# Performance work log

Hardware: AMD Instinct MI355X
Metric: run time of the kernel (lower is better)

Reference implementation:

```python
import jax, jax.numpy as jnp
import numpy as np

N_NODES = 100000
N_EDGES = 1600000
NODE_DIM = 128
EDGE_DIM = 32
GLOBAL_DIM = 64
HIDDEN_DIM = 256
N_GRAPHS = 512
IN_DIM = NODE_DIM + EDGE_DIM + GLOBAL_DIM  # 224


def setup_inputs() -> dict:
    key = jax.random.key(0)
    ks = jax.random.split(key, 10)
    x = jax.random.normal(ks[0], (N_NODES, NODE_DIM), dtype=jnp.float32)
    edge_index = jax.random.randint(ks[1], (2, N_EDGES), 0, N_NODES, dtype=jnp.int64)
    edge_attr = jax.random.normal(ks[2], (N_EDGES, EDGE_DIM), dtype=jnp.float32)
    u = jax.random.normal(ks[3], (N_GRAPHS, GLOBAL_DIM), dtype=jnp.float32)
    batch = jnp.sort(jax.random.randint(ks[4], (N_NODES,), 0, N_GRAPHS, dtype=jnp.int64))
    s1 = 1.0 / np.sqrt(IN_DIM)
    s2 = 1.0 / np.sqrt(HIDDEN_DIM)
    W1 = jax.random.uniform(ks[5], (IN_DIM, HIDDEN_DIM), jnp.float32, -s1, s1)
    b1 = jnp.zeros((HIDDEN_DIM,), jnp.float32)
    W2 = jax.random.uniform(ks[6], (HIDDEN_DIM, HIDDEN_DIM), jnp.float32, -s2, s2)
    b2 = jnp.zeros((HIDDEN_DIM,), jnp.float32)
    W3 = jax.random.uniform(ks[7], (HIDDEN_DIM, GLOBAL_DIM), jnp.float32, -s2, s2)
    b3 = jnp.zeros((GLOBAL_DIM,), jnp.float32)
    return {"x": x, "edge_index": edge_index, "edge_attr": edge_attr, "u": u,
            "batch": batch, "W1": W1, "b1": b1, "W2": W2, "b2": b2, "W3": W3, "b3": b3}


def _scatter_mean(vals, seg_ids, num_segments):
    # vals: [M, D], seg_ids: [M] -> [num_segments, D]
    sums = jax.ops.segment_sum(vals, seg_ids, num_segments=num_segments)
    cnt = jax.ops.segment_sum(jnp.ones((vals.shape[0],), vals.dtype), seg_ids,
                              num_segments=num_segments)
    return sums / jnp.maximum(cnt, 1.0)[:, None]


def reference(x, edge_index, edge_attr, u, batch, W1, b1, W2, b2, W3, b3):
    B = u.shape[0]
    node_mean = _scatter_mean(x, batch, B)                      # [B, node_dim]
    edge_seg = batch[edge_index[0]]                             # [E]
    edge_mean = _scatter_mean(edge_attr, edge_seg, B)           # [B, edge_dim]
    out = jnp.concatenate([node_mean, edge_mean, u], axis=1)    # [B, in_dim]
    h = jax.nn.relu(out @ W1 + b1)
    h = jax.nn.relu(h @ W2 + b2)
    return h @ W3 + b3                                          # [B, global_dim]
```

## Files before the change

### kernel.cpp

```cpp
#include <hip/hip_runtime.h>
#include <hip/hip_bf16.h>

#define N_NODES    100000
#define N_EDGES    1600000
#define NODE_DIM   128
#define EDGE_DIM   32
#define GLOBAL_DIM 64
#define HIDDEN_DIM 256
#define N_GRAPHS   512
#define IN_DIM     224
#define ROW33      33

#define EDGE_BLKS  256
#define EDGE_CH    (N_EDGES / EDGE_BLKS)
#define SLOTSZ     (N_GRAPHS * ROW33)
#define GPB        2
#define PD         4

#define FXS   1048576.0f
#define FXINV (1.0f / 1048576.0f)

#define WS_NSUM   0
#define WS_NCNT   (WS_NSUM + N_GRAPHS * NODE_DIM)
#define WS_ESLOT  (WS_NCNT + N_GRAPHS)

__global__ __launch_bounds__(1024, 8) void bulk(const float* __restrict__ eattr,
                                                const int* __restrict__ eidx,
                                                const float* __restrict__ x,
                                                const int* __restrict__ batch,
                                                int* __restrict__ eslot,
                                                float* __restrict__ nsum,
                                                float* __restrict__ ncnt) {
    __shared__ int ssum[SLOTSZ];
    const int t = threadIdx.x;

    if (blockIdx.x < EDGE_BLKS) {
        for (int i = t; i < SLOTSZ; i += 1024) ssum[i] = 0;
        __syncthreads();

        const float4* eattr4 = reinterpret_cast<const float4*>(eattr);
        const int p  = t & 7;
        const int e0 = blockIdx.x * EDGE_CH + (t >> 3);
        const int e1 = blockIdx.x * EDGE_CH + EDGE_CH;

        int    sQ[PD];
        float4 vQ[PD];
        int    iQ[PD];
#pragma unroll
        for (int k = 0; k < PD; ++k) {
            const int ek = e0 + k * 128;
            const int idx = eidx[ek];
            sQ[k] = batch[idx];
            vQ[k] = eattr4[(size_t)ek * 8 + p];
            iQ[k] = eidx[min(ek + PD * 128, N_EDGES - 1)];
        }

        for (int e = e0; e < e1; e += PD * 128) {
#pragma unroll
            for (int k = 0; k < PD; ++k) {
                const int ek = e + k * 128;
                if (ek < e1) {
                    const int s = sQ[k];
                    const float4 v = vQ[k];
                    const int ef = ek + PD * 128;
                    sQ[k] = batch[iQ[k]];
                    vQ[k] = (ef < e1) ? eattr4[(size_t)ef * 8 + p]
                                      : float4{0.f, 0.f, 0.f, 0.f};
                    iQ[k] = eidx[min(ek + 2 * PD * 128, N_EDGES - 1)];
                    const int b = s * ROW33 + p * 4;
                    atomicAdd(&ssum[b + 0], __float2int_rn(v.x * FXS));
                    atomicAdd(&ssum[b + 1], __float2int_rn(v.y * FXS));
                    atomicAdd(&ssum[b + 2], __float2int_rn(v.z * FXS));
                    atomicAdd(&ssum[b + 3], __float2int_rn(v.w * FXS));
                    if (p == 0) atomicAdd(&ssum[s * ROW33 + 32], 1);
                }
            }
        }
        __syncthreads();

        int* gs = eslot + (size_t)blockIdx.x * SLOTSZ;
        for (int i = t; i < SLOTSZ; i += 1024) gs[i] = ssum[i];
    } else {
        const int g = blockIdx.x - EDGE_BLKS;
        __shared__ int sb[2];
        if (t < 2) {
            const int target = g + t;
            int lo = 0, hi = N_NODES;
            while (lo < hi) {
                const int mid = (lo + hi) >> 1;
                if (batch[mid] < target) lo = mid + 1; else hi = mid;
            }
            sb[t] = lo;
        }
        __syncthreads();
        const int s0 = sb[0], e0 = sb[1];

        const int dq = t & 31;
        const int off = t >> 5;
        float4 a0 = float4{0.f, 0.f, 0.f, 0.f}, a1 = a0;
        int r = s0 + off;
        for (; r + 32 < e0; r += 64) {
            const float4 v0 = *reinterpret_cast<const float4*>(x + (size_t)(r     ) * NODE_DIM + dq * 4);
            const float4 v1 = *reinterpret_cast<const float4*>(x + (size_t)(r + 32) * NODE_DIM + dq * 4);
            a0.x += v0.x; a0.y += v0.y; a0.z += v0.z; a0.w += v0.w;
            a1.x += v1.x; a1.y += v1.y; a1.z += v1.z; a1.w += v1.w;
        }
        for (; r < e0; r += 32) {
            const float4 v = *reinterpret_cast<const float4*>(x + (size_t)r * NODE_DIM + dq * 4);
            a0.x += v.x; a0.y += v.y; a0.z += v.z; a0.w += v.w;
        }
        a0.x += a1.x; a0.y += a1.y; a0.z += a1.z; a0.w += a1.w;

        float4* part4 = reinterpret_cast<float4*>(ssum);
        part4[t] = a0;
        __syncthreads();
        if (t < 32) {
            float4 s = float4{0.f, 0.f, 0.f, 0.f};
#pragma unroll 32
            for (int k = 0; k < 32; ++k) {
                const float4 v = part4[t + 32 * k];
                s.x += v.x; s.y += v.y; s.z += v.z; s.w += v.w;
            }
            reinterpret_cast<float4*>(nsum)[(size_t)g * 32 + t] = s;
        }
        if (t == 0) ncnt[g] = fmaxf((float)(e0 - s0), 1.f);
    }
}

__global__ __launch_bounds__(256) void finalize_mlp(const float* __restrict__ nsum,
                                                    const float* __restrict__ ncnt,
                                                    const int* __restrict__ eslot,
                                                    const float* __restrict__ u,
                                                    const float* __restrict__ W1, const float* __restrict__ b1,
                                                    const float* __restrict__ W2, const float* __restrict__ b2,
                                                    const float* __restrict__ W3, const float* __restrict__ b3,
                                                    float* __restrict__ out) {
    const int g0 = blockIdx.x * GPB;
    const int t = threadIdx.x;
    __shared__ float fs[GPB * IN_DIM];
    __shared__ long long redll[256];
    __shared__ long long redcnt[8];
    __shared__ float h[GPB][HIDDEN_DIM];
    __shared__ float h2[GPB][HIDDEN_DIM];
    __shared__ float red[GPB][256];
    __shared__ float s_ecnt[GPB];

    {
        const int col = t & 63, part = t >> 6;
        const int g = col >> 5, d = col & 31;
        long long s = 0;
#pragma unroll 8
        for (int sl = part * 64; sl < part * 64 + 64; ++sl)
            s += eslot[(size_t)sl * SLOTSZ + (size_t)(g0 + g) * ROW33 + d];
        redll[t] = s;
    }
    if (t < 8) {
        const int g = t & 1, part = t >> 1;
        long long c = 0;
#pragma unroll 8
        for (int sl = part * 64; sl < part * 64 + 64; ++sl)
            c += eslot[(size_t)sl * SLOTSZ + (size_t)(g0 + g) * ROW33 + 32];
        redcnt[t] = c;
    }
    __syncthreads();
    if (t < GPB)
        s_ecnt[t] = fmaxf((float)(redcnt[t] + redcnt[t + 2] + redcnt[t + 4] + redcnt[t + 6]), 1.f);

    {
        const int g = t >> 7, d = t & 127;
        fs[g * IN_DIM + d] = nsum[(size_t)(g0 + g) * NODE_DIM + d] / ncnt[g0 + g];
    }
    __syncthreads();
    if (t < 64) {
        const long long tot = redll[t] + redll[t + 64] + redll[t + 128] + redll[t + 192];
        const int g = t >> 5, d = t & 31;
        fs[g * IN_DIM + NODE_DIM + d] = ((float)tot * FXINV) / s_ecnt[g];
    } else if (t < 192) {
        const int i = t - 64, g = i >> 6, c = i & 63;
        fs[g * IN_DIM + NODE_DIM + EDGE_DIM + c] = u[(size_t)(g0 + g) * GLOBAL_DIM + c];
    }
    __syncthreads();

    float acc0, acc1;
    const float bb1 = b1[t];
    acc0 = acc1 = bb1;
    for (int k = 0; k < IN_DIM; ++k) {
        const float w = W1[k * HIDDEN_DIM + t];
        acc0 = fmaf(fs[k], w, acc0);
        acc1 = fmaf(fs[IN_DIM + k], w, acc1);
    }
    h[0][t] = fmaxf(acc0, 0.f); h[1][t] = fmaxf(acc1, 0.f);
    __syncthreads();

    const float bb2 = b2[t];
    acc0 = acc1 = bb2;
    for (int k = 0; k < HIDDEN_DIM; ++k) {
        const float w = W2[k * HIDDEN_DIM + t];
        acc0 = fmaf(h[0][k], w, acc0);
        acc1 = fmaf(h[1][k], w, acc1);
    }
    h2[0][t] = fmaxf(acc0, 0.f); h2[1][t] = fmaxf(acc1, 0.f);
    __syncthreads();

    const int c3 = t & 63, q = t >> 6;
    acc0 = acc1 = 0.f;
    for (int k = q * 64; k < q * 64 + 64; ++k) {
        const float w = W3[k * GLOBAL_DIM + c3];
        acc0 = fmaf(h2[0][k], w, acc0);
        acc1 = fmaf(h2[1][k], w, acc1);
    }
    red[0][t] = acc0; red[1][t] = acc1;
    __syncthreads();
    if (t < GPB * GLOBAL_DIM) {
        const int g = t >> 6, c = t & 63;
        out[(size_t)(g0 + g) * GLOBAL_DIM + c] = red[g][c] + red[g][c + 64] +
                                                 red[g][c + 128] + red[g][c + 192] + b3[c];
    }
}

extern "C" void kernel_launch(void* const* d_in, const int* in_sizes, int n_in,
                              void* d_out, int out_size, void* d_ws, size_t ws_size,
                              hipStream_t stream) {
    const float* x         = (const float*)d_in[0];
    const int*   edge_idx  = (const int*)d_in[1];
    const float* edge_attr = (const float*)d_in[2];
    const float* u         = (const float*)d_in[3];
    const int*   batch     = (const int*)d_in[4];
    const float* W1 = (const float*)d_in[5];
    const float* b1 = (const float*)d_in[6];
    const float* W2 = (const float*)d_in[7];
    const float* b2 = (const float*)d_in[8];
    const float* W3 = (const float*)d_in[9];
    const float* b3 = (const float*)d_in[10];
    float* out = (float*)d_out;

    int* ws32 = (int*)d_ws;
    float* nsum  = (float*)(ws32 + WS_NSUM);
    float* ncnt  = (float*)(ws32 + WS_NCNT);
    int*   eslot = ws32 + WS_ESLOT;

    bulk<<<EDGE_BLKS + N_GRAPHS, 1024, 0, stream>>>(edge_attr, edge_idx, x, batch,
                                                    eslot, nsum, ncnt);
    finalize_mlp<<<N_GRAPHS / GPB, 256, 0, stream>>>(nsum, ncnt, eslot, u,
                                                     W1, b1, W2, b2, W3, b3, out);
}
```

Before: 81.35 us.

## Stage per-edge segment ids in LDS before edge accumulation loop

Each edge block now first resolves batch[eidx[e]] for its whole chunk with coalesced, independent gathers and stores the segment ids as 16-bit values in shared memory. The main loop then reads segment ids from LDS and only streams edge attributes, replacing the hand-rolled register prefetch queue with a simple unrolled loop. This separates the dependent two-level gather from the atomic accumulation so the gather latency is not exposed in the hot loop. In exchange it adds about 12.5 KB of LDS per block, an extra barrier phase, and drops the occupancy hint from launch bounds.

Result: slower. 84.28 us (+3.6%).

```diff
diff --git a/kernel.cpp b/kernel.cpp
--- a/kernel.cpp
+++ b/kernel.cpp
@@ -15,7 +15,6 @@
 #define EDGE_CH    (N_EDGES / EDGE_BLKS)
 #define SLOTSZ     (N_GRAPHS * ROW33)
 #define GPB        2
-#define PD         4
 
 #define FXS   1048576.0f
 #define FXINV (1.0f / 1048576.0f)
@@ -24,57 +23,37 @@
 #define WS_NCNT   (WS_NSUM + N_GRAPHS * NODE_DIM)
 #define WS_ESLOT  (WS_NCNT + N_GRAPHS)
 
-__global__ __launch_bounds__(1024, 8) void bulk(const float* __restrict__ eattr,
-                                                const int* __restrict__ eidx,
-                                                const float* __restrict__ x,
-                                                const int* __restrict__ batch,
-                                                int* __restrict__ eslot,
-                                                float* __restrict__ nsum,
-                                                float* __restrict__ ncnt) {
+__global__ __launch_bounds__(1024) void bulk(const float* __restrict__ eattr,
+                                             const int* __restrict__ eidx,
+                                             const float* __restrict__ x,
+                                             const int* __restrict__ batch,
+                                             int* __restrict__ eslot,
+                                             float* __restrict__ nsum,
+                                             float* __restrict__ ncnt) {
     __shared__ int ssum[SLOTSZ];
+    __shared__ unsigned short seg_lds[EDGE_CH];
     const int t = threadIdx.x;
 
     if (blockIdx.x < EDGE_BLKS) {
+        const int ebase = blockIdx.x * EDGE_CH;
+
         for (int i = t; i < SLOTSZ; i += 1024) ssum[i] = 0;
+        for (int i = t; i < EDGE_CH; i += 1024)
+            seg_lds[i] = (unsigned short)batch[eidx[ebase + i]];
         __syncthreads();
 
         const float4* eattr4 = reinterpret_cast<const float4*>(eattr);
-        const int p  = t & 7;
-        const int e0 = blockIdx.x * EDGE_CH + (t >> 3);
-        const int e1 = blockIdx.x * EDGE_CH + EDGE_CH;
-
-        int    sQ[PD];
-        float4 vQ[PD];
-        int    iQ[PD];
-#pragma unroll
-        for (int k = 0; k < PD; ++k) {
-            const int ek = e0 + k * 128;
-            const int idx = eidx[ek];
-            sQ[k] = batch[idx];
-            vQ[k] = eattr4[(size_t)ek * 8 + p];
-            iQ[k] = eidx[min(ek + PD * 128, N_EDGES - 1)];
-        }
-
-        for (int e = e0; e < e1; e += PD * 128) {
-#pragma unroll
-            for (int k = 0; k < PD; ++k) {
-                const int ek = e + k * 128;
-                if (ek < e1) {
-                    const int s = sQ[k];
-                    const float4 v = vQ[k];
-                    const int ef = ek + PD * 128;
-                    sQ[k] = batch[iQ[k]];
-                    vQ[k] = (ef < e1) ? eattr4[(size_t)ef * 8 + p]
-                                      : float4{0.f, 0.f, 0.f, 0.f};
-                    iQ[k] = eidx[min(ek + 2 * PD * 128, N_EDGES - 1)];
-                    const int b = s * ROW33 + p * 4;
-                    atomicAdd(&ssum[b + 0], __float2int_rn(v.x * FXS));
-                    atomicAdd(&ssum[b + 1], __float2int_rn(v.y * FXS));
-                    atomicAdd(&ssum[b + 2], __float2int_rn(v.z * FXS));
-                    atomicAdd(&ssum[b + 3], __float2int_rn(v.w * FXS));
-                    if (p == 0) atomicAdd(&ssum[s * ROW33 + 32], 1);
-                }
-            }
+        const int p = t & 7;
+#pragma unroll 4
+        for (int i = (t >> 3); i < EDGE_CH; i += 128) {
+            const int s = seg_lds[i];
+            const float4 v = eattr4[(size_t)(ebase + i) * 8 + p];
+            const int b = s * ROW33 + p * 4;
+            atomicAdd(&ssum[b + 0], __float2int_rn(v.x * FXS));
+            atomicAdd(&ssum[b + 1], __float2int_rn(v.y * FXS));
+            atomicAdd(&ssum[b + 2], __float2int_rn(v.z * FXS));
+            atomicAdd(&ssum[b + 3], __float2int_rn(v.w * FXS));
+            if (p == 0) atomicAdd(&ssum[s * ROW33 + 32], 1);
         }
         __syncthreads();
 
```
